# Kernel optimization log

Measured on AMD Instinct MI355X. Metric: run time of the kernel, lower is better.

Reference implementation:

```python
import jax, jax.numpy as jnp
import numpy as np

EPS = 1e-7          # self.eps[float32]
MIN_NORM = 1e-15
PROJ_EPS = 4e-3     # PoincareBall proj epsilon (float32)
FD_R = 2.0          # args.r
FD_T = 1.0          # args.t
DIS_CLIP = 40.0     # args.dis_mx_clip
ATT_BETA = 0.2      # args.att_beta
# curvature c = 1.0 (self.cur = [1.0, ...]); sqrt_c = 1 so it is folded out below.

def _norm(x):
    return jnp.maximum(jnp.linalg.norm(x, axis=-1, keepdims=True), MIN_NORM)

def expmap0(u):
    n = _norm(u)
    return jnp.tanh(n) * u / n

def proj(x):
    n = _norm(x)
    maxnorm = 1.0 - PROJ_EPS
    return jnp.where(n > maxnorm, x / n * maxnorm, x)

def proj_tan0_exp(u):
    return proj(expmap0(u))

def artanh(x):
    x = jnp.clip(x, -1.0 + EPS, 1.0 - EPS)
    return 0.5 * (jnp.log1p(x) - jnp.log1p(-x))

def mobius_add(x, y):
    x2 = jnp.sum(x * x, -1, keepdims=True)
    y2 = jnp.sum(y * y, -1, keepdims=True)
    xy = jnp.sum(x * y, -1, keepdims=True)
    num = (1.0 + 2.0 * xy + y2) * x + (1.0 - x2) * y
    den = 1.0 + 2.0 * xy + x2 * y2
    return num / jnp.maximum(den, MIN_NORM)

def sqdist(p, q):
    d = 2.0 * artanh(jnp.linalg.norm(mobius_add(-p, q), axis=-1))
    return d * d

def to_klein(x):
    return 2.0 * x / (1.0 + jnp.sum(x * x, -1, keepdims=True))

def lorentz_factor(x):
    return 1.0 / jnp.sqrt(jnp.maximum(1.0 - jnp.sum(x * x, -1), EPS))

def klein_to(x):
    return x / (1.0 + jnp.sqrt(jnp.maximum(1.0 - jnp.sum(x * x, -1, keepdims=True), EPS)))

N_ENTITY, N_REL, DIM = 200000, 32, 64
B, H, M = 1024, 2, 32

def setup_inputs() -> dict:
    key = jax.random.key(0)
    ks = jax.random.split(key, 9)
    return {
        'users': jax.random.randint(ks[0], (B,), 0, 10000),
        'items': jax.random.randint(ks[1], (B,), 0, N_ENTITY),
        'labels': jax.random.randint(ks[2], (B,), 0, 2),
        'mem_h': jax.random.randint(ks[3], (H, B, M), 0, N_ENTITY),
        'mem_r': jax.random.randint(ks[4], (H, B, M), 0, N_REL),
        'mem_t': jax.random.randint(ks[5], (H, B, M), 0, N_ENTITY),
        'entity_emb': 0.05 * jax.random.normal(ks[6], (N_ENTITY, DIM), dtype=jnp.float32),
        'rela_plus_emb': 0.05 * jax.random.normal(ks[7], (N_REL, DIM), dtype=jnp.float32),
        'relation_emb': 0.1 * jax.random.normal(ks[8], (N_REL, DIM * DIM), dtype=jnp.float32),
    }

def reference(users, items, labels, mem_h, mem_r, mem_t,
              entity_emb, rela_plus_emb, relation_emb):
    d = entity_emb.shape[-1]
    item = entity_emb[items]                                  # [B, d]
    h = entity_emb[mem_h]                                     # [H, B, M, d]
    t = entity_emb[mem_t]                                     # [H, B, M, d]
    R = relation_emb[mem_r].reshape(*mem_r.shape, d, d) / 10.0  # [H, B, M, d, d]
    # relation-transform of heads, mapped to the Poincare ball (dropout=eval/identity)
    Rh = proj_tan0_exp(jnp.einsum('hbmij,hbmj->hbmi', R, h))  # [H, B, M, d]
    hyp_item = proj(proj_tan0_exp(item))                      # [B, d] (res = proj(hyp_item))
    dist2 = sqdist(Rh, hyp_item[None, :, None, :])            # [H, B, M]
    att = jnp.exp(-ATT_BETA * dist2 - 0.05)
    kle_t = to_klein(proj_tan0_exp(t))                        # [H, B, M, d]
    p1 = lorentz_factor(kle_t) * att                          # [H, B, M]
    w1 = p1 / jnp.maximum(jnp.sum(p1, -1, keepdims=True), EPS)
    kle_o = jnp.einsum('hbm,hbmd->bhd', w1, kle_t)            # [B, H, d]
    # hop aggregation (one_like_bahop is all-ones)
    p2 = lorentz_factor(kle_o)                                # [B, H]
    w2 = p2 / jnp.maximum(jnp.sum(p2, -1, keepdims=True), EPS)
    o = jnp.einsum('bh,bhd->bd', w2, kle_o)                   # [B, d]
    hyp_o = proj(klein_to(o))
    d2 = sqdist(hyp_o, proj_tan0_exp(item))                   # [B]
    scores = 1.0 / (jnp.exp(jnp.minimum(d2 - FD_R, DIS_CLIP) / FD_T) + 1.0)
    return scores
```

## Files before the change

### kernel.cpp

```cpp
#include <hip/hip_runtime.h>
#include <hip/hip_bf16.h>

#define DIMV 64

static constexpr float F_EPS  = 1e-7f;
static constexpr float F_MINN = 1e-15f;
static constexpr float F_MAXN = 1.0f - 4e-3f;

__device__ __forceinline__ float frcp(float x) { return __builtin_amdgcn_rcpf(x); }
__device__ __forceinline__ float frsq(float x) { return __builtin_amdgcn_rsqf(x); }
__device__ __forceinline__ float tanh_fast(float x) {
    float e = __expf(2.0f * x);
    return 1.0f - 2.0f * frcp(e + 1.0f);
}

__device__ __forceinline__ float wave_sum1(float v) {
#pragma unroll
    for (int off = 32; off > 0; off >>= 1) v += __shfl_xor(v, off, 64);
    return v;
}
__device__ __forceinline__ void wave_sum2(float& a, float& b) {
#pragma unroll
    for (int off = 32; off > 0; off >>= 1) {
        a += __shfl_xor(a, off, 64);
        b += __shfl_xor(b, off, 64);
    }
}
__device__ __forceinline__ void wave_sum3(float& a, float& b, float& c) {
#pragma unroll
    for (int off = 32; off > 0; off >>= 1) {
        a += __shfl_xor(a, off, 64);
        b += __shfl_xor(b, off, 64);
        c += __shfl_xor(c, off, 64);
    }
}

__global__ void k_hist(const int* __restrict__ mr, int n, int* __restrict__ hist) {
    __shared__ int lh[32];
    if (threadIdx.x < 32) lh[threadIdx.x] = 0;
    __syncthreads();
    for (int i = blockIdx.x * blockDim.x + threadIdx.x; i < n; i += gridDim.x * blockDim.x)
        atomicAdd(&lh[mr[i]], 1);
    __syncthreads();
    if (threadIdx.x < 32 && lh[threadIdx.x]) atomicAdd(&hist[threadIdx.x], lh[threadIdx.x]);
}

__global__ void k_scan(const int* __restrict__ hist, int* __restrict__ cursor) {
    if (threadIdx.x == 0) {
        int acc = 0;
        for (int r = 0; r < 32; ++r) { cursor[r] = acc; acc += hist[r]; }
    }
}

__global__ void k_scatter(const int* __restrict__ mr, int n,
                          int* __restrict__ cursor, int* __restrict__ bins) {
    __shared__ int lcnt[32], lbase[32];
    const int tid = threadIdx.x;
    if (tid < 32) lcnt[tid] = 0;
    __syncthreads();
    int idxA[4], rnkA[4], relA[4];
    int cnt = 0;
    int i = blockIdx.x * blockDim.x + tid;
#pragma unroll
    for (int kk = 0; kk < 4; ++kk) {
        if (i < n) {
            int r = mr[i];
            idxA[kk] = i; relA[kk] = r;
            rnkA[kk] = atomicAdd(&lcnt[r], 1);
            cnt = kk + 1;
        }
        i += gridDim.x * blockDim.x;
    }
    __syncthreads();
    if (tid < 32) lbase[tid] = atomicAdd(&cursor[tid], lcnt[tid]);
    __syncthreads();
#pragma unroll
    for (int kk = 0; kk < 4; ++kk)
        if (kk < cnt) bins[lbase[relA[kk]] + rnkA[kk]] = idxA[kk];
}

__global__ __launch_bounds__(256) void k_q(const int* __restrict__ items,
                                           const float* __restrict__ ent,
                                           float* __restrict__ qbuf,
                                           float* __restrict__ y2buf, int B) {
    const int wave = threadIdx.x >> 6, lane = threadIdx.x & 63;
    const int b = blockIdx.x * 4 + wave;
    if (b >= B) return;
    const int it = items[b];
    const float iv = ent[(long)it * DIMV + lane];
    float n2 = wave_sum1(iv * iv);
    float n  = fmaxf(sqrtf(n2), F_MINN);
    float te = tanh_fast(n);
    float s  = (te > F_MAXN) ? F_MAXN * frcp(te) : 1.0f;
    qbuf[(long)b * DIMV + lane] = iv * (te * frcp(n)) * s;
    if (lane == 0) { float qn = te * s; y2buf[b] = qn * qn; }
}

template<int MM, int BB>
__global__ __launch_bounds__(256, 4) void k_main(
        const int*   __restrict__ mem_h,
        const int*   __restrict__ mem_r,
        const int*   __restrict__ mem_t,
        const float* __restrict__ ent,
        const float* __restrict__ rel,
        const int*   __restrict__ bins,
        const float* __restrict__ qbuf,
        const float* __restrict__ y2buf,
        float2*      __restrict__ pkbuf,
        int M, int B, int ntask, int per_wave)
{
    const int lane = threadIdx.x & 63;
    const int wid  = blockIdx.x * 4 + (threadIdx.x >> 6);
    const int start = wid * per_wave;

    float4 r0, r1, r2, r3, r4, r5, r6, r7, r8, r9, r10, r11, r12, r13, r14, r15;
    int cur_r = -1;

    for (int k = 0; k < per_wave; ++k) {
        const int idx = start + k;
        if (idx >= ntask) return;
        const int t = __builtin_amdgcn_readfirstlane(bins[idx]);
        const int r = __builtin_amdgcn_readfirstlane(mem_r[t]);
        if (r != cur_r) {
            const float4* Rp = (const float4*)(rel + (long)r * (DIMV * DIMV)) + lane * 16;
            r0  = Rp[0];  r1  = Rp[1];  r2  = Rp[2];  r3  = Rp[3];
            r4  = Rp[4];  r5  = Rp[5];  r6  = Rp[6];  r7  = Rp[7];
            r8  = Rp[8];  r9  = Rp[9];  r10 = Rp[10]; r11 = Rp[11];
            r12 = Rp[12]; r13 = Rp[13]; r14 = Rp[14]; r15 = Rp[15];
            cur_r = r;
        }
        const int ih  = __builtin_amdgcn_readfirstlane(mem_h[t]);
        const int itt = __builtin_amdgcn_readfirstlane(mem_t[t]);
        const int b   = MM ? ((t / MM) & (BB - 1))
                           : (int)(((unsigned)t / (unsigned)M) % (unsigned)B);

        const float* hp = ent + (long)ih * DIMV;
        const float  tv = ent[(long)itt * DIMV + lane];
        const float  q  = qbuf[(long)b * DIMV + lane];
        const float  y2 = y2buf[b];

        float u0 = 0.f, u1 = 0.f, u2 = 0.f, u3 = 0.f;
#define STEP(J, RV) \
        u0 = fmaf(RV.x, hp[4 * (J) + 0], u0); \
        u1 = fmaf(RV.y, hp[4 * (J) + 1], u1); \
        u2 = fmaf(RV.z, hp[4 * (J) + 2], u2); \
        u3 = fmaf(RV.w, hp[4 * (J) + 3], u3);
        STEP(0, r0)  STEP(1, r1)  STEP(2, r2)  STEP(3, r3)
        STEP(4, r4)  STEP(5, r5)  STEP(6, r6)  STEP(7, r7)
        STEP(8, r8)  STEP(9, r9)  STEP(10, r10) STEP(11, r11)
        STEP(12, r12) STEP(13, r13) STEP(14, r14) STEP(15, r15)
#undef STEP
        const float u = ((u0 + u1) + (u2 + u3)) * 0.1f;

        float uu = u * u, uq = u * q, tt = tv * tv;
        wave_sum3(uu, uq, tt);

        float nu = fmaxf(sqrtf(uu), F_MINN);
        float te = tanh_fast(nu);
        float sc = (te > F_MAXN) ? F_MAXN * frcp(te) : 1.0f;
        float pn = te * sc;
        float x2 = pn * pn;
        float xy = -(pn * frcp(nu)) * uq;

        float A_  = 1.0f + 2.0f * xy + y2;
        float B_  = 1.0f - x2;
        float nm2 = fmaxf(A_ * A_ * x2 + B_ * B_ * y2 + 2.0f * A_ * B_ * xy, 0.0f);
        float den = fmaxf(1.0f + 2.0f * xy + x2 * y2, 1e-15f);
        float v   = fminf(sqrtf(nm2) * frcp(den), 1.0f - F_EPS);
        float dd  = __logf((1.0f + v) * frcp(1.0f - v));
        float att = __expf(fmaf(-0.2f, dd * dd, -0.05f));

        float nt  = fmaxf(sqrtf(tt), F_MINN);
        float tte = tanh_fast(nt);
        float ts  = (tte > F_MAXN) ? F_MAXN * frcp(tte) : 1.0f;
        float ptn = tte * ts;
        float a2  = ptn * ptn;
        float i1a = frcp(1.0f + a2);
        float kn2 = 4.0f * a2 * i1a * i1a;
        float lf  = frsq(fmaxf(1.0f - kn2, F_EPS));
        float p1  = lf * att;
        float kfc = 2.0f * ptn * frcp(nt) * i1a;

        if (lane == 0) pkbuf[t] = make_float2(p1, kfc);
    }
}

__global__ __launch_bounds__(256) void k_agg(
        const int*    __restrict__ mem_t,
        const float*  __restrict__ ent,
        const float2* __restrict__ pkbuf,
        const float*  __restrict__ qbuf,
        const float*  __restrict__ y2buf,
        float*        __restrict__ out,
        int B, int M)
{
    const int b    = blockIdx.x;
    const int wave = threadIdx.x >> 6;
    const int lane = threadIdx.x & 63;
    const int h    = wave >> 1;
    const int mhalf = M >> 1;
    const int mst  = (wave & 1) * mhalf;

    float accA = 0.0f, accS = 0.0f;
    const long ibase = ((long)h * B + b) * M + mst;

#pragma unroll 4
    for (int k = 0; k < mhalf; ++k) {
        const long t  = ibase + k;
        const int itt = __builtin_amdgcn_readfirstlane(mem_t[t]);
        const float2 pk = pkbuf[t];
        const float  tv = ent[(long)itt * DIMV + lane];
        accS += pk.x;
        accA = fmaf(pk.x * pk.y, tv, accA);
    }

    __shared__ float A_l[4][DIMV];
    __shared__ float S_l[4];
    A_l[wave][lane] = accA;
    if (lane == 0) S_l[wave] = accS;
    __syncthreads();

    if (wave == 0) {
        const float q  = qbuf[(long)b * DIMV + lane];
        const float y2 = y2buf[b];

        float k0 = (A_l[0][lane] + A_l[1][lane]) * frcp(fmaxf(S_l[0] + S_l[1], F_EPS));
        float k1 = (A_l[2][lane] + A_l[3][lane]) * frcp(fmaxf(S_l[2] + S_l[3], F_EPS));
        float n0 = k0 * k0, n1 = k1 * k1;
        wave_sum2(n0, n1);
        float p20 = frsq(fmaxf(1.0f - n0, F_EPS));
        float p21 = frsq(fmaxf(1.0f - n1, F_EPS));
        float o   = (p20 * k0 + p21 * k1) * frcp(fmaxf(p20 + p21, F_EPS));

        float oo = o * o, oq = o * q;
        wave_sum2(oo, oq);
        float kd    = 1.0f + sqrtf(fmaxf(1.0f - oo, F_EPS));
        float invkd = frcp(kd);
        float ko2   = oo * invkd * invkd;
        float nk    = fmaxf(sqrtf(ko2), F_MINN);
        float ps    = (nk > F_MAXN) ? F_MAXN * frcp(nk) : 1.0f;
        float x2    = (nk * ps) * (nk * ps);
        float xy    = -(ps * invkd) * oq;

        float A_  = 1.0f + 2.0f * xy + y2;
        float B_  = 1.0f - x2;
        float nm2 = fmaxf(A_ * A_ * x2 + B_ * B_ * y2 + 2.0f * A_ * B_ * xy, 0.0f);
        float den = fmaxf(1.0f + 2.0f * xy + x2 * y2, 1e-15f);
        float v   = fminf(sqrtf(nm2) * frcp(den), 1.0f - F_EPS);
        float dd  = __logf((1.0f + v) * frcp(1.0f - v));
        float d2  = dd * dd;

        float scr = frcp(__expf(fminf(d2 - 2.0f, 40.0f)) + 1.0f);
        if (lane == 0) out[b] = scr;
    }
}

extern "C" void kernel_launch(void* const* d_in, const int* in_sizes, int n_in,
                              void* d_out, int out_size, void* d_ws, size_t ws_size,
                              hipStream_t stream) {
    const int*   items = (const int*)d_in[1];
    const int*   mh    = (const int*)d_in[3];
    const int*   mr    = (const int*)d_in[4];
    const int*   mt    = (const int*)d_in[5];
    const float* ent   = (const float*)d_in[6];
    const float* rel   = (const float*)d_in[8];
    float* out = (float*)d_out;

    const int B = in_sizes[1];
    const int n = in_sizes[3];
    const int M = n / (2 * B);

    float*  qbuf   = (float*)d_ws;
    float*  y2buf  = qbuf + (size_t)B * DIMV;
    float2* pkbuf  = (float2*)(y2buf + B);
    int*    hist   = (int*)((float*)pkbuf + 2 * (size_t)n);
    int*    cursor = hist + 32;
    int*    bins   = cursor + 32;

    hipMemsetAsync(hist, 0, 32 * sizeof(int), stream);
    k_hist<<<dim3(64), dim3(256), 0, stream>>>(mr, n, hist);
    k_scan<<<dim3(1), dim3(64), 0, stream>>>(hist, cursor);
    {
        int g = (n + 1023) / 1024;
        k_scatter<<<dim3(g), dim3(256), 0, stream>>>(mr, n, cursor, bins);
    }
    k_q<<<dim3((B + 3) / 4), dim3(256), 0, stream>>>(items, ent, qbuf, y2buf, B);

    const int per_wave = 16;
    const int g_main = (n + per_wave * 4 - 1) / (per_wave * 4);
    if (M == 32 && B == 1024)
        k_main<32, 1024><<<dim3(g_main), dim3(256), 0, stream>>>(
            mh, mr, mt, ent, rel, bins, qbuf, y2buf, pkbuf, M, B, n, per_wave);
    else
        k_main<0, 0><<<dim3(g_main), dim3(256), 0, stream>>>(
            mh, mr, mt, ent, rel, bins, qbuf, y2buf, pkbuf, M, B, n, per_wave);

    k_agg<<<dim3(B), dim3(256), 0, stream>>>(mt, ent, pkbuf, qbuf, y2buf, out, B, M);
}
```

Before: 162.6 us.

## Fuse tail aggregation into main kernel via atomics and relation-aligned work chunks

Builds a schedule of chunks, each holding up to 16 tasks that share one relation, so every wave loads the 64x64 relation matrix into registers exactly once. The main kernel now accumulates p1*kfc*t and p1 directly into per-(h,b) slots with global atomics. This removes the pkbuf round trip and the second pass that re-gathered tail embeddings in k_agg, and a light k_fin kernel computes the final scores. The cost is heavy atomic contention on 65 floats per (h,b), a larger memset, and a summation order that is no longer deterministic.

```diff
diff --git a/kernel.cpp b/kernel.cpp
--- a/kernel.cpp
+++ b/kernel.cpp
@@ -2,6 +2,9 @@
 #include <hip/hip_bf16.h>
 
 #define DIMV 64
+#define PW   16
+
+typedef float f32x4 __attribute__((ext_vector_type(4)));
 
 static constexpr float F_EPS  = 1e-7f;
 static constexpr float F_MINN = 1e-15f;
@@ -45,11 +48,26 @@
     if (threadIdx.x < 32 && lh[threadIdx.x]) atomicAdd(&hist[threadIdx.x], lh[threadIdx.x]);
 }
 
-__global__ void k_scan(const int* __restrict__ hist, int* __restrict__ cursor) {
-    if (threadIdx.x == 0) {
-        int acc = 0;
-        for (int r = 0; r < 32; ++r) { cursor[r] = acc; acc += hist[r]; }
-    }
+__global__ void k_sched(const int* __restrict__ hist, int* __restrict__ cursor,
+                        int2* __restrict__ sched, int* __restrict__ nsched) {
+    const int lane = threadIdx.x;
+    int cnt = (lane < 32) ? hist[lane] : 0;
+    int nch = (cnt + PW - 1) / PW;
+    int ic = cnt, in = nch;
+#pragma unroll
+    for (int off = 1; off < 32; off <<= 1) {
+        int a = __shfl_up(ic, off, 64);
+        int b = __shfl_up(in, off, 64);
+        if (lane >= off) { ic += a; in += b; }
+    }
+    const int binstart = ic - cnt;
+    const int chbase   = in - nch;
+    if (lane < 32) {
+        cursor[lane] = binstart;
+        for (int c = 0; c < nch; ++c)
+            sched[chbase + c] = make_int2(binstart + c * PW, min(PW, cnt - c * PW));
+    }
+    if (lane == 31) *nsched = in;
 }
 
 __global__ void k_scatter(const int* __restrict__ mr, int n,
@@ -104,35 +122,41 @@
         const float* __restrict__ ent,
         const float* __restrict__ rel,
         const int*   __restrict__ bins,
+        const int2*  __restrict__ sched,
+        const int*   __restrict__ nsched,
         const float* __restrict__ qbuf,
         const float* __restrict__ y2buf,
-        float2*      __restrict__ pkbuf,
-        int M, int B, int ntask, int per_wave)
+        float*       __restrict__ acc,
+        int M, int B)
 {
     const int lane = threadIdx.x & 63;
     const int wid  = blockIdx.x * 4 + (threadIdx.x >> 6);
-    const int start = wid * per_wave;
-
-    float4 r0, r1, r2, r3, r4, r5, r6, r7, r8, r9, r10, r11, r12, r13, r14, r15;
-    int cur_r = -1;
-
-    for (int k = 0; k < per_wave; ++k) {
-        const int idx = start + k;
-        if (idx >= ntask) return;
-        const int t = __builtin_amdgcn_readfirstlane(bins[idx]);
-        const int r = __builtin_amdgcn_readfirstlane(mem_r[t]);
-        if (r != cur_r) {
-            const float4* Rp = (const float4*)(rel + (long)r * (DIMV * DIMV)) + lane * 16;
-            r0  = Rp[0];  r1  = Rp[1];  r2  = Rp[2];  r3  = Rp[3];
-            r4  = Rp[4];  r5  = Rp[5];  r6  = Rp[6];  r7  = Rp[7];
-            r8  = Rp[8];  r9  = Rp[9];  r10 = Rp[10]; r11 = Rp[11];
-            r12 = Rp[12]; r13 = Rp[13]; r14 = Rp[14]; r15 = Rp[15];
-            cur_r = r;
-        }
+    const int ns   = __builtin_amdgcn_readfirstlane(*nsched);
+    if (wid >= ns) return;
+
+    const int2 e    = sched[wid];
+    const int start = __builtin_amdgcn_readfirstlane(e.x);
+    const int count = __builtin_amdgcn_readfirstlane(e.y);
+
+    const int r0t = __builtin_amdgcn_readfirstlane(bins[start]);
+    const int r   = __builtin_amdgcn_readfirstlane(mem_r[r0t]);
+    const f32x4* Rp = (const f32x4*)(rel + (long)r * (DIMV * DIMV)) + lane * 16;
+    f32x4 r0  = Rp[0],  r1  = Rp[1],  r2  = Rp[2],  r3  = Rp[3];
+    f32x4 r4  = Rp[4],  r5  = Rp[5],  r6  = Rp[6],  r7  = Rp[7];
+    f32x4 r8  = Rp[8],  r9  = Rp[9],  r10 = Rp[10], r11 = Rp[11];
+    f32x4 r12 = Rp[12], r13 = Rp[13], r14 = Rp[14], r15 = Rp[15];
+
+    for (int k = 0; k < count; ++k) {
+        asm volatile("" : "+v"(r0), "+v"(r1), "+v"(r2), "+v"(r3),
+                          "+v"(r4), "+v"(r5), "+v"(r6), "+v"(r7),
+                          "+v"(r8), "+v"(r9), "+v"(r10), "+v"(r11),
+                          "+v"(r12), "+v"(r13), "+v"(r14), "+v"(r15));
+
+        const int t   = __builtin_amdgcn_readfirstlane(bins[start + k]);
         const int ih  = __builtin_amdgcn_readfirstlane(mem_h[t]);
         const int itt = __builtin_amdgcn_readfirstlane(mem_t[t]);
-        const int b   = MM ? ((t / MM) & (BB - 1))
-                           : (int)(((unsigned)t / (unsigned)M) % (unsigned)B);
+        const int hb  = MM ? (t / MM) : (int)((unsigned)t / (unsigned)M);
+        const int b   = BB ? (hb & (BB - 1)) : (hb % B);
 
         const float* hp = ent + (long)ih * DIMV;
         const float  tv = ent[(long)itt * DIMV + lane];
@@ -145,9 +169,9 @@
         u1 = fmaf(RV.y, hp[4 * (J) + 1], u1); \
         u2 = fmaf(RV.z, hp[4 * (J) + 2], u2); \
         u3 = fmaf(RV.w, hp[4 * (J) + 3], u3);
-        STEP(0, r0)  STEP(1, r1)  STEP(2, r2)  STEP(3, r3)
-        STEP(4, r4)  STEP(5, r5)  STEP(6, r6)  STEP(7, r7)
-        STEP(8, r8)  STEP(9, r9)  STEP(10, r10) STEP(11, r11)
+        STEP(0, r0)   STEP(1, r1)   STEP(2, r2)   STEP(3, r3)
+        STEP(4, r4)   STEP(5, r5)   STEP(6, r6)   STEP(7, r7)
+        STEP(8, r8)   STEP(9, r9)   STEP(10, r10) STEP(11, r11)
         STEP(12, r12) STEP(13, r13) STEP(14, r14) STEP(15, r15)
 #undef STEP
         const float u = ((u0 + u1) + (u2 + u3)) * 0.1f;
@@ -181,78 +205,57 @@
         float p1  = lf * att;
         float kfc = 2.0f * ptn * frcp(nt) * i1a;
 
-        if (lane == 0) pkbuf[t] = make_float2(p1, kfc);
-    }
-}
-
-__global__ __launch_bounds__(256) void k_agg(
-        const int*    __restrict__ mem_t,
-        const float*  __restrict__ ent,
-        const float2* __restrict__ pkbuf,
-        const float*  __restrict__ qbuf,
-        const float*  __restrict__ y2buf,
-        float*        __restrict__ out,
-        int B, int M)
+        float* slot = acc + (long)hb * 65;
+        atomicAdd(slot + lane, p1 * kfc * tv);
+        if (lane == 0) atomicAdd(slot + 64, p1);
+    }
+}
+
+__global__ __launch_bounds__(256) void k_fin(
+        const float* __restrict__ acc,
+        const float* __restrict__ qbuf,
+        const float* __restrict__ y2buf,
+        float*       __restrict__ out,
+        int B)
 {
-    const int b    = blockIdx.x;
-    const int wave = threadIdx.x >> 6;
-    const int lane = threadIdx.x & 63;
-    const int h    = wave >> 1;
-    const int mhalf = M >> 1;
-    const int mst  = (wave & 1) * mhalf;
-
-    float accA = 0.0f, accS = 0.0f;
-    const long ibase = ((long)h * B + b) * M + mst;
-
-#pragma unroll 4
-    for (int k = 0; k < mhalf; ++k) {
-        const long t  = ibase + k;
-        const int itt = __builtin_amdgcn_readfirstlane(mem_t[t]);
-        const float2 pk = pkbuf[t];
-        const float  tv = ent[(long)itt * DIMV + lane];
-        accS += pk.x;
-        accA = fmaf(pk.x * pk.y, tv, accA);
-    }
-
-    __shared__ float A_l[4][DIMV];
-    __shared__ float S_l[4];
-    A_l[wave][lane] = accA;
-    if (lane == 0) S_l[wave] = accS;
-    __syncthreads();
-
-    if (wave == 0) {
-        const float q  = qbuf[(long)b * DIMV + lane];
-        const float y2 = y2buf[b];
-
-        float k0 = (A_l[0][lane] + A_l[1][lane]) * frcp(fmaxf(S_l[0] + S_l[1], F_EPS));
-        float k1 = (A_l[2][lane] + A_l[3][lane]) * frcp(fmaxf(S_l[2] + S_l[3], F_EPS));
-        float n0 = k0 * k0, n1 = k1 * k1;
-        wave_sum2(n0, n1);
-        float p20 = frsq(fmaxf(1.0f - n0, F_EPS));
-        float p21 = frsq(fmaxf(1.0f - n1, F_EPS));
-        float o   = (p20 * k0 + p21 * k1) * frcp(fmaxf(p20 + p21, F_EPS));
-
-        float oo = o * o, oq = o * q;
-        wave_sum2(oo, oq);
-        float kd    = 1.0f + sqrtf(fmaxf(1.0f - oo, F_EPS));
-        float invkd = frcp(kd);
-        float ko2   = oo * invkd * invkd;
-        float nk    = fmaxf(sqrtf(ko2), F_MINN);
-        float ps    = (nk > F_MAXN) ? F_MAXN * frcp(nk) : 1.0f;
-        float x2    = (nk * ps) * (nk * ps);
-        float xy    = -(ps * invkd) * oq;
-
-        float A_  = 1.0f + 2.0f * xy + y2;
-        float B_  = 1.0f - x2;
-        float nm2 = fmaxf(A_ * A_ * x2 + B_ * B_ * y2 + 2.0f * A_ * B_ * xy, 0.0f);
-        float den = fmaxf(1.0f + 2.0f * xy + x2 * y2, 1e-15f);
-        float v   = fminf(sqrtf(nm2) * frcp(den), 1.0f - F_EPS);
-        float dd  = __logf((1.0f + v) * frcp(1.0f - v));
-        float d2  = dd * dd;
-
-        float scr = frcp(__expf(fminf(d2 - 2.0f, 40.0f)) + 1.0f);
-        if (lane == 0) out[b] = scr;
-    }
+    const int wave = threadIdx.x >> 6, lane = threadIdx.x & 63;
+    const int b = blockIdx.x * 4 + wave;
+    if (b >= B) return;
+
+    const float q  = qbuf[(long)b * DIMV + lane];
+    const float y2 = y2buf[b];
+
+    const float* s0 = acc + (long)b * 65;
+    const float* s1 = acc + (long)(B + b) * 65;
+    float k0 = s0[lane] * frcp(fmaxf(s0[64], F_EPS));
+    float k1 = s1[lane] * frcp(fmaxf(s1[64], F_EPS));
+
+    float n0 = k0 * k0, n1 = k1 * k1;
+    wave_sum2(n0, n1);
+    float p20 = frsq(fmaxf(1.0f - n0, F_EPS));
+    float p21 = frsq(fmaxf(1.0f - n1, F_EPS));
+    float o   = (p20 * k0 + p21 * k1) * frcp(fmaxf(p20 + p21, F_EPS));
+
+    float oo = o * o, oq = o * q;
+    wave_sum2(oo, oq);
+    float kd    = 1.0f + sqrtf(fmaxf(1.0f - oo, F_EPS));
+    float invkd = frcp(kd);
+    float ko2   = oo * invkd * invkd;
+    float nk    = fmaxf(sqrtf(ko2), F_MINN);
+    float ps    = (nk > F_MAXN) ? F_MAXN * frcp(nk) : 1.0f;
+    float x2    = (nk * ps) * (nk * ps);
+    float xy    = -(ps * invkd) * oq;
+
+    float A_  = 1.0f + 2.0f * xy + y2;
+    float B_  = 1.0f - x2;
+    float nm2 = fmaxf(A_ * A_ * x2 + B_ * B_ * y2 + 2.0f * A_ * B_ * xy, 0.0f);
+    float den = fmaxf(1.0f + 2.0f * xy + x2 * y2, 1e-15f);
+    float v   = fminf(sqrtf(nm2) * frcp(den), 1.0f - F_EPS);
+    float dd  = __logf((1.0f + v) * frcp(1.0f - v));
+    float d2  = dd * dd;
+
+    float scr = frcp(__expf(fminf(d2 - 2.0f, 40.0f)) + 1.0f);
+    if (lane == 0) out[b] = scr;
 }
 
 extern "C" void kernel_launch(void* const* d_in, const int* in_sizes, int n_in,
@@ -269,31 +272,34 @@
     const int B = in_sizes[1];
     const int n = in_sizes[3];
     const int M = n / (2 * B);
-
-    float*  qbuf   = (float*)d_ws;
-    float*  y2buf  = qbuf + (size_t)B * DIMV;
-    float2* pkbuf  = (float2*)(y2buf + B);
-    int*    hist   = (int*)((float*)pkbuf + 2 * (size_t)n);
-    int*    cursor = hist + 32;
-    int*    bins   = cursor + 32;
-
-    hipMemsetAsync(hist, 0, 32 * sizeof(int), stream);
+    const int maxe = (n + PW - 1) / PW + 32;
+
+    int*   hist   = (int*)d_ws;
+    int*   cursor = hist + 32;
+    float* acc    = (float*)(cursor + 32);
+    size_t zero_bytes = 64 * sizeof(int) + (size_t)2 * B * 65 * sizeof(float);
+    int*   nsched = (int*)((char*)d_ws + zero_bytes);
+    int2*  sched  = (int2*)(nsched + 1);
+    int*   bins   = (int*)(sched + maxe);
+    float* qbuf   = (float*)(bins + n);
+    float* y2buf  = qbuf + (size_t)B * DIMV;
+
+    hipMemsetAsync(d_ws, 0, zero_bytes, stream);
     k_hist<<<dim3(64), dim3(256), 0, stream>>>(mr, n, hist);
-    k_scan<<<dim3(1), dim3(64), 0, stream>>>(hist, cursor);
+    k_sched<<<dim3(1), dim3(64), 0, stream>>>(hist, cursor, sched, nsched);
     {
         int g = (n + 1023) / 1024;
         k_scatter<<<dim3(g), dim3(256), 0, stream>>>(mr, n, cursor, bins);
     }
     k_q<<<dim3((B + 3) / 4), dim3(256), 0, stream>>>(items, ent, qbuf, y2buf, B);
 
-    const int per_wave = 16;
-    const int g_main = (n + per_wave * 4 - 1) / (per_wave * 4);
+    const int g_main = (maxe + 3) / 4;
     if (M == 32 && B == 1024)
         k_main<32, 1024><<<dim3(g_main), dim3(256), 0, stream>>>(
-            mh, mr, mt, ent, rel, bins, qbuf, y2buf, pkbuf, M, B, n, per_wave);
+            mh, mr, mt, ent, rel, bins, sched, nsched, qbuf, y2buf, acc, M, B);
     else
         k_main<0, 0><<<dim3(g_main), dim3(256), 0, stream>>>(
-            mh, mr, mt, ent, rel, bins, qbuf, y2buf, pkbuf, M, B, n, per_wave);
-
-    k_agg<<<dim3(B), dim3(256), 0, stream>>>(mt, ent, pkbuf, qbuf, y2buf, out, B, M);
-}
+            mh, mr, mt, ent, rel, bins, sched, nsched, qbuf, y2buf, acc, M, B);
+
+    k_fin<<<dim3((B + 3) / 4), dim3(256), 0, stream>>>(acc, qbuf, y2buf, out, B);
+}
```

Measured after the change: 167.9 us. +3.3%, slower.
